# Kernel tuning notes

Measured on AMD Instinct MI355X. Metric: run time of the kernel, lower is better.

Reference implementation:

```python
import jax, jax.numpy as jnp
import numpy as np


def setup_inputs() -> dict:
    key = jax.random.key(0)
    k1, k2, k3, k4 = jax.random.split(key, 4)
    B, C, H, W = 4, 256, 48, 48
    scale = 1.0 / np.sqrt(C)  # conv-like init scale
    x = jax.random.normal(k1, (B, C, H, W), dtype=jnp.float32)
    wq = jax.random.normal(k2, (C, C), dtype=jnp.float32) * scale
    wk = jax.random.normal(k3, (C, C), dtype=jnp.float32) * scale
    wv = jax.random.normal(k4, (C, C), dtype=jnp.float32) * scale
    return {"x": x, "wq": wq, "wk": wk, "wv": wv}


def reference(x, wq, wk, wv):
    B, C, H, W = x.shape
    num_heads = 8
    d_k = C // num_heads
    N = H * W

    # 1x1 convs (bias=False) are channel-mixing matmuls: [out_c, in_c]
    def proj(w):
        y = jnp.einsum('oc,bchw->bohw', w, x)
        # view(B, heads, d_k, H*W)
        return y.reshape(B, num_heads, d_k, N)

    q = proj(wq)  # [B, h, d_k, N]
    k = proj(wk)
    v = proj(wv)

    # scores = q^T k / sqrt(d_k) -> [B, h, N, N]
    scores = jnp.einsum('bhdn,bhdm->bhnm', q, k) / jnp.sqrt(jnp.asarray(d_k, x.dtype))
    attn = jax.nn.softmax(scores, axis=-1)
    # out = attn @ v^T -> [B, h, N, d_k]
    out = jnp.einsum('bhnm,bhdm->bhnd', attn, v)
    # permute back to [B, h, d_k, N] then view(B, C, H, W)
    out = out.transpose(0, 1, 3, 2).reshape(B, C, H, W)
    return x + out
```

## Files before the change

### kernel.cpp

```cpp
#include <hip/hip_runtime.h>

constexpr int B  = 4;
constexpr int C  = 256;
constexpr int N  = 2304;
constexpr int NH = 8;
constexpr int DK = 32;

typedef short short8 __attribute__((ext_vector_type(8)));
typedef float f32x4  __attribute__((ext_vector_type(4)));

static __device__ __forceinline__ ushort f2bf(float f) {
    union { float f; unsigned u; } v; v.f = f;
    unsigned r = (v.u + 0x7FFFu + ((v.u >> 16) & 1u)) >> 16;
    return (ushort)r;
}

__global__ __launch_bounds__(256) void proj_kernel(
    const float* __restrict__ x,
    const float* __restrict__ wq,
    const float* __restrict__ wk,
    const float* __restrict__ wv,
    ushort* __restrict__ ws,
    int bfix, size_t matStride, size_t batchStride)
{
    const int tile = blockIdx.x;
    const int mat  = blockIdx.y;
    const int b    = (bfix >= 0) ? bfix : (int)blockIdx.z;
    const int nt = tile % (N / 64);
    const int ot = tile / (N / 64);
    const int n0 = nt * 64;
    const int o0 = ot * 64;

    const float* w = (mat == 0) ? wq : (mat == 1) ? wk : wv;
    ushort* out = ws + (size_t)mat * matStride + (size_t)b * batchStride;
    const float* xb = x + (size_t)b * C * N;

    __shared__ float xs[16][64];
    __shared__ float wt[64][17];

    const int tid = threadIdx.x;
    const int tx = tid & 15;
    const int ty = tid >> 4;

    float acc[4][4] = {};

    for (int k0 = 0; k0 < C; k0 += 16) {
        {
            const int kk  = tid >> 4;
            const int nn4 = tid & 15;
            float4 v = *reinterpret_cast<const float4*>(xb + (size_t)(k0 + kk) * N + n0 + nn4 * 4);
            *reinterpret_cast<float4*>(&xs[kk][nn4 * 4]) = v;
        }
        {
            const int oo = tid >> 2;
            const int k4 = tid & 3;
            float4 v = *reinterpret_cast<const float4*>(w + (size_t)(o0 + oo) * C + k0 + k4 * 4);
            wt[oo][k4 * 4 + 0] = v.x;
            wt[oo][k4 * 4 + 1] = v.y;
            wt[oo][k4 * 4 + 2] = v.z;
            wt[oo][k4 * 4 + 3] = v.w;
        }
        __syncthreads();

        #pragma unroll
        for (int kk = 0; kk < 16; ++kk) {
            float4 a = *reinterpret_cast<const float4*>(&xs[kk][tx * 4]);
            float av[4] = {a.x, a.y, a.z, a.w};
            float bv[4];
            #pragma unroll
            for (int jo = 0; jo < 4; ++jo) bv[jo] = wt[ty * 4 + jo][kk];
            #pragma unroll
            for (int jo = 0; jo < 4; ++jo)
                #pragma unroll
                for (int jn = 0; jn < 4; ++jn)
                    acc[jo][jn] = fmaf(bv[jo], av[jn], acc[jo][jn]);
        }
        __syncthreads();
    }

    const float sc = (mat == 0) ? 0.17677669529663687f : 1.0f;
    #pragma unroll
    for (int jn = 0; jn < 4; ++jn) {
        ushort4 wv4 = make_ushort4(f2bf(acc[0][jn] * sc), f2bf(acc[1][jn] * sc),
                                   f2bf(acc[2][jn] * sc), f2bf(acc[3][jn] * sc));
        *reinterpret_cast<ushort4*>(out + (size_t)(n0 + tx * 4 + jn) * C + o0 + ty * 4) = wv4;
    }
}

__global__ __launch_bounds__(256) void attn_kernel(
    const ushort* __restrict__ ws,
    const float* __restrict__ x,
    float* __restrict__ out,
    int bfix, size_t matStride, size_t batchStride, int ppx)
{
    __shared__ __align__(16) char smem[18944];
    ushort* Ks  = (ushort*)smem;
    ushort* Vt  = (ushort*)(smem + 5120);
    float*  Ost = (float*) smem;

    const int tid = threadIdx.x;
    const int wq = tid >> 6;
    const int l  = tid & 63;
    const int lq = l & 15;
    const int g  = l >> 4;

    ushort* Pl = (ushort*)(smem + 9728) + wq * 1152;

    const int gid  = blockIdx.x;
    const int xcd  = gid & 7;
    const int loc  = gid >> 3;
    const int pair = xcd * ppx + loc / 36;
    const int qt   = loc % 36;
    const int h    = pair & 7;
    const int b    = (bfix >= 0) ? bfix : (pair >> 3);
    const int n0   = qt * 64;

    const ushort* qb = ws + (size_t)b * batchStride;
    const ushort* kb = qb + matStride;
    const ushort* vb = qb + 2 * matStride;

    short8 qf = *reinterpret_cast<const short8*>(
        qb + (size_t)(n0 + wq * 16 + lq) * C + h * DK + 8 * g);

    f32x4 acc0 = {0.f, 0.f, 0.f, 0.f};
    f32x4 acc1 = {0.f, 0.f, 0.f, 0.f};
    float m = -1e30f, lsum = 0.f;

    const int srow = tid >> 2, sch = tid & 3;
    const int kp = tid & 31, dg = tid >> 5;

    for (int m0 = 0; m0 < N; m0 += 64) {
        *reinterpret_cast<short8*>(Ks + srow * 40 + sch * 8) =
            *reinterpret_cast<const short8*>(kb + (size_t)(m0 + srow) * C + h * DK + sch * 8);
        {
            const ushort* v0 = vb + (size_t)(m0 + 2 * kp) * C + h * DK + dg * 4;
            ushort4 a  = *reinterpret_cast<const ushort4*>(v0);
            ushort4 c4 = *reinterpret_cast<const ushort4*>(v0 + C);
            *reinterpret_cast<unsigned*>(Vt + (dg * 4 + 0) * 72 + 2 * kp) = (unsigned)a.x | ((unsigned)c4.x << 16);
            *reinterpret_cast<unsigned*>(Vt + (dg * 4 + 1) * 72 + 2 * kp) = (unsigned)a.y | ((unsigned)c4.y << 16);
            *reinterpret_cast<unsigned*>(Vt + (dg * 4 + 2) * 72 + 2 * kp) = (unsigned)a.z | ((unsigned)c4.z << 16);
            *reinterpret_cast<unsigned*>(Vt + (dg * 4 + 3) * 72 + 2 * kp) = (unsigned)a.w | ((unsigned)c4.w << 16);
        }
        __syncthreads();

        f32x4 st[4];
        #pragma unroll
        for (int t = 0; t < 4; ++t) {
            short8 kf = *reinterpret_cast<const short8*>(Ks + (lq + 16 * t) * 40 + 8 * g);
            f32x4 z = {0.f, 0.f, 0.f, 0.f};
            st[t] = __builtin_amdgcn_mfma_f32_16x16x32_bf16(kf, qf, z, 0, 0, 0);
        }

        float mx = st[0][0];
        #pragma unroll
        for (int t = 0; t < 4; ++t)
            #pragma unroll
            for (int r = 0; r < 4; ++r) mx = fmaxf(mx, st[t][r]);
        mx = fmaxf(mx, __shfl_xor(mx, 16));
        mx = fmaxf(mx, __shfl_xor(mx, 32));
        const float newm = fmaxf(m, mx);
        const float corr = __expf(m - newm);
        m = newm;

        float ps = 0.f;
        ushort pb[16];
        #pragma unroll
        for (int t = 0; t < 4; ++t)
            #pragma unroll
            for (int r = 0; r < 4; ++r) {
                float p = __expf(st[t][r] - m);
                ps += p;
                pb[t * 4 + r] = f2bf(p);
            }
        ps += __shfl_xor(ps, 16);
        ps += __shfl_xor(ps, 32);
        lsum = lsum * corr + ps;

        float cw[4];
        #pragma unroll
        for (int r = 0; r < 4; ++r) cw[r] = __shfl(corr, 4 * g + r);
        #pragma unroll
        for (int r = 0; r < 4; ++r) { acc0[r] *= cw[r]; acc1[r] *= cw[r]; }

        #pragma unroll
        for (int t = 0; t < 4; ++t) {
            ushort4 w4 = make_ushort4(pb[4 * t], pb[4 * t + 1], pb[4 * t + 2], pb[4 * t + 3]);
            *reinterpret_cast<ushort4*>(Pl + lq * 72 + 4 * g + 16 * t) = w4;
        }

        short8 pf0 = *reinterpret_cast<const short8*>(Pl + lq * 72 + 8 * g);
        short8 pf1 = *reinterpret_cast<const short8*>(Pl + lq * 72 + 32 + 8 * g);
        #pragma unroll
        for (int kc = 0; kc < 2; ++kc) {
            short8 pf = kc ? pf1 : pf0;
            short8 vf0 = *reinterpret_cast<const short8*>(Vt + lq * 72 + 32 * kc + 8 * g);
            short8 vf1 = *reinterpret_cast<const short8*>(Vt + (lq + 16) * 72 + 32 * kc + 8 * g);
            acc0 = __builtin_amdgcn_mfma_f32_16x16x32_bf16(pf, vf0, acc0, 0, 0, 0);
            acc1 = __builtin_amdgcn_mfma_f32_16x16x32_bf16(pf, vf1, acc1, 0, 0, 0);
        }
        __syncthreads();
    }

    const float iv = 1.0f / lsum;
    float iw[4];
    #pragma unroll
    for (int r = 0; r < 4; ++r) iw[r] = __shfl(iv, 4 * g + r);
    #pragma unroll
    for (int r = 0; r < 4; ++r) {
        Ost[(lq +  0) * 68 + wq * 16 + 4 * g + r] = acc0[r] * iw[r];
        Ost[(lq + 16) * 68 + wq * 16 + 4 * g + r] = acc1[r] * iw[r];
    }
    __syncthreads();

    {
        const int d  = tid >> 3;
        const int nn = (tid & 7) * 8;
        const size_t go = ((size_t)b * C + h * DK + d) * (size_t)N + n0 + nn;
        float4 o1 = *reinterpret_cast<float4*>(Ost + d * 68 + nn);
        float4 o2 = *reinterpret_cast<float4*>(Ost + d * 68 + nn + 4);
        float4 x1 = *reinterpret_cast<const float4*>(x + go);
        float4 x2 = *reinterpret_cast<const float4*>(x + go + 4);
        *reinterpret_cast<float4*>(out + go)     = make_float4(o1.x + x1.x, o1.y + x1.y, o1.z + x1.z, o1.w + x1.w);
        *reinterpret_cast<float4*>(out + go + 4) = make_float4(o2.x + x2.x, o2.y + x2.y, o2.z + x2.z, o2.w + x2.w);
    }
}

extern "C" void kernel_launch(void* const* d_in, const int* in_sizes, int n_in,
                              void* d_out, int out_size, void* d_ws, size_t ws_size,
                              hipStream_t stream) {
    const float* x  = (const float*)d_in[0];
    const float* wq = (const float*)d_in[1];
    const float* wk = (const float*)d_in[2];
    const float* wv = (const float*)d_in[3];
    float* out = (float*)d_out;
    ushort* ws = (ushort*)d_ws;

    const size_t NC = (size_t)N * C;
    const size_t needFull = 3 * (size_t)B * NC * sizeof(ushort);

    if (ws_size >= needFull) {
        proj_kernel<<<dim3((N / 64) * (C / 64), 3, B), 256, 0, stream>>>(
            x, wq, wk, wv, ws, -1, (size_t)B * NC, NC);
        attn_kernel<<<dim3(36 * NH * B), 256, 0, stream>>>(
            ws, x, out, -1, (size_t)B * NC, NC, 4);
    } else {
        for (int b = 0; b < B; ++b) {
            proj_kernel<<<dim3((N / 64) * (C / 64), 3, 1), 256, 0, stream>>>(
                x, wq, wk, wv, ws, b, NC, 0);
            attn_kernel<<<dim3(36 * NH), 256, 0, stream>>>(
                ws, x, out, b, NC, 0, 1);
        }
    }
}
```

Before: 232.1 us.

## Shrink attention blocks, prefetch K/V tiles into registers, use exp2 with lazy rescaling

The attention kernel now uses 128-thread blocks covering 32 queries each, which doubles the grid and cuts shared memory per block. The next K/V tile is loaded into registers while the current one is computed, and MFMA sections are wrapped in s_setprio. The softmax switches to exp2 by folding log2(e) into the Q scale, rescales the running max only when a wave's max grows by more than 8, defers the lsum reduction to the end, and uses the v_cvt_pk_bf16_f32 packed convert. In exchange, K/V are read from global once per 32 queries instead of once per 64, doubling that traffic, and the lazy rescale lets intermediate values grow by up to 2^8.

Measured after the change: 229.6 us. No clear change (-1.0%).

```diff
diff --git a/kernel.cpp b/kernel.cpp
--- a/kernel.cpp
+++ b/kernel.cpp
@@ -11,8 +11,12 @@
 
 static __device__ __forceinline__ ushort f2bf(float f) {
     union { float f; unsigned u; } v; v.f = f;
-    unsigned r = (v.u + 0x7FFFu + ((v.u >> 16) & 1u)) >> 16;
-    return (ushort)r;
+    return (ushort)((v.u + 0x7FFFu + ((v.u >> 16) & 1u)) >> 16);
+}
+static __device__ __forceinline__ unsigned cvtpk(float lo, float hi) {
+    unsigned r;
+    asm("v_cvt_pk_bf16_f32 %0, %1, %2" : "=v"(r) : "v"(lo), "v"(hi));
+    return r;
 }
 
 __global__ __launch_bounds__(256) void proj_kernel(
@@ -26,10 +30,8 @@
     const int tile = blockIdx.x;
     const int mat  = blockIdx.y;
     const int b    = (bfix >= 0) ? bfix : (int)blockIdx.z;
-    const int nt = tile % (N / 64);
-    const int ot = tile / (N / 64);
-    const int n0 = nt * 64;
-    const int o0 = ot * 64;
+    const int n0 = (tile % (N / 64)) * 64;
+    const int o0 = (tile / (N / 64)) * 64;
 
     const float* w = (mat == 0) ? wq : (mat == 1) ? wk : wv;
     ushort* out = ws + (size_t)mat * matStride + (size_t)b * batchStride;
@@ -78,7 +80,7 @@
         __syncthreads();
     }
 
-    const float sc = (mat == 0) ? 0.17677669529663687f : 1.0f;
+    const float sc = (mat == 0) ? 0.25503450535f : 1.0f;
     #pragma unroll
     for (int jn = 0; jn < 4; ++jn) {
         ushort4 wv4 = make_ushort4(f2bf(acc[0][jn] * sc), f2bf(acc[1][jn] * sc),
@@ -87,33 +89,33 @@
     }
 }
 
-__global__ __launch_bounds__(256) void attn_kernel(
+__global__ __launch_bounds__(128) void attn_kernel(
     const ushort* __restrict__ ws,
     const float* __restrict__ x,
     float* __restrict__ out,
     int bfix, size_t matStride, size_t batchStride, int ppx)
 {
-    __shared__ __align__(16) char smem[18944];
+    __shared__ __align__(16) char smem[14336];
     ushort* Ks  = (ushort*)smem;
     ushort* Vt  = (ushort*)(smem + 5120);
     float*  Ost = (float*) smem;
 
     const int tid = threadIdx.x;
-    const int wq = tid >> 6;
-    const int l  = tid & 63;
-    const int lq = l & 15;
-    const int g  = l >> 4;
+    const int wq  = tid >> 6;
+    const int l   = tid & 63;
+    const int lq  = l & 15;
+    const int g   = l >> 4;
 
     ushort* Pl = (ushort*)(smem + 9728) + wq * 1152;
 
     const int gid  = blockIdx.x;
     const int xcd  = gid & 7;
     const int loc  = gid >> 3;
-    const int pair = xcd * ppx + loc / 36;
-    const int qt   = loc % 36;
+    const int pair = xcd * ppx + loc / 72;
+    const int qt   = loc % 72;
     const int h    = pair & 7;
     const int b    = (bfix >= 0) ? bfix : (pair >> 3);
-    const int n0   = qt * 64;
+    const int n0   = qt * 32;
 
     const ushort* qb = ws + (size_t)b * batchStride;
     const ushort* kb = qb + matStride;
@@ -126,98 +128,139 @@
     f32x4 acc1 = {0.f, 0.f, 0.f, 0.f};
     float m = -1e30f, lsum = 0.f;
 
-    const int srow = tid >> 2, sch = tid & 3;
-    const int kp = tid & 31, dg = tid >> 5;
-
-    for (int m0 = 0; m0 < N; m0 += 64) {
-        *reinterpret_cast<short8*>(Ks + srow * 40 + sch * 8) =
-            *reinterpret_cast<const short8*>(kb + (size_t)(m0 + srow) * C + h * DK + sch * 8);
+    const int kr = tid >> 2, kc = tid & 3;
+    const int vp = tid & 31, vd = tid >> 5;
+
+    short8  kreg0, kreg1;
+    ushort4 va0, vc0, va1, vc1;
+
+    #define LOAD_TILE(m0_)                                                          \
+        {                                                                           \
+            const int m0i = (m0_);                                                  \
+            kreg0 = *reinterpret_cast<const short8*>(kb + (size_t)(m0i + kr) * C + h * DK + kc * 8);        \
+            kreg1 = *reinterpret_cast<const short8*>(kb + (size_t)(m0i + 32 + kr) * C + h * DK + kc * 8);   \
+            const ushort* v0 = vb + (size_t)(m0i + 2 * vp) * C + h * DK + vd * 4;   \
+            va0 = *reinterpret_cast<const ushort4*>(v0);                            \
+            vc0 = *reinterpret_cast<const ushort4*>(v0 + C);                        \
+            va1 = *reinterpret_cast<const ushort4*>(v0 + 16);                       \
+            vc1 = *reinterpret_cast<const ushort4*>(v0 + C + 16);                   \
+        }
+
+    LOAD_TILE(0);
+
+    for (int t = 0; t < N / 64; ++t) {
+        *reinterpret_cast<short8*>(Ks + kr * 40 + kc * 8) = kreg0;
+        *reinterpret_cast<short8*>(Ks + (kr + 32) * 40 + kc * 8) = kreg1;
         {
-            const ushort* v0 = vb + (size_t)(m0 + 2 * kp) * C + h * DK + dg * 4;
-            ushort4 a  = *reinterpret_cast<const ushort4*>(v0);
-            ushort4 c4 = *reinterpret_cast<const ushort4*>(v0 + C);
-            *reinterpret_cast<unsigned*>(Vt + (dg * 4 + 0) * 72 + 2 * kp) = (unsigned)a.x | ((unsigned)c4.x << 16);
-            *reinterpret_cast<unsigned*>(Vt + (dg * 4 + 1) * 72 + 2 * kp) = (unsigned)a.y | ((unsigned)c4.y << 16);
-            *reinterpret_cast<unsigned*>(Vt + (dg * 4 + 2) * 72 + 2 * kp) = (unsigned)a.z | ((unsigned)c4.z << 16);
-            *reinterpret_cast<unsigned*>(Vt + (dg * 4 + 3) * 72 + 2 * kp) = (unsigned)a.w | ((unsigned)c4.w << 16);
-        }
-        __syncthreads();
+            unsigned p0 = (unsigned)va0.x | ((unsigned)vc0.x << 16);
+            unsigned p1 = (unsigned)va0.y | ((unsigned)vc0.y << 16);
+            unsigned p2 = (unsigned)va0.z | ((unsigned)vc0.z << 16);
+            unsigned p3 = (unsigned)va0.w | ((unsigned)vc0.w << 16);
+            *reinterpret_cast<unsigned*>(Vt + (vd * 4 + 0) * 72 + 2 * vp) = p0;
+            *reinterpret_cast<unsigned*>(Vt + (vd * 4 + 1) * 72 + 2 * vp) = p1;
+            *reinterpret_cast<unsigned*>(Vt + (vd * 4 + 2) * 72 + 2 * vp) = p2;
+            *reinterpret_cast<unsigned*>(Vt + (vd * 4 + 3) * 72 + 2 * vp) = p3;
+            unsigned q0 = (unsigned)va1.x | ((unsigned)vc1.x << 16);
+            unsigned q1 = (unsigned)va1.y | ((unsigned)vc1.y << 16);
+            unsigned q2 = (unsigned)va1.z | ((unsigned)vc1.z << 16);
+            unsigned q3 = (unsigned)va1.w | ((unsigned)vc1.w << 16);
+            *reinterpret_cast<unsigned*>(Vt + (vd * 4 + 16) * 72 + 2 * vp) = q0;
+            *reinterpret_cast<unsigned*>(Vt + (vd * 4 + 17) * 72 + 2 * vp) = q1;
+            *reinterpret_cast<unsigned*>(Vt + (vd * 4 + 18) * 72 + 2 * vp) = q2;
+            *reinterpret_cast<unsigned*>(Vt + (vd * 4 + 19) * 72 + 2 * vp) = q3;
+        }
+        __syncthreads();
+
+        if (t < N / 64 - 1) LOAD_TILE((t + 1) * 64);
 
         f32x4 st[4];
-        #pragma unroll
-        for (int t = 0; t < 4; ++t) {
-            short8 kf = *reinterpret_cast<const short8*>(Ks + (lq + 16 * t) * 40 + 8 * g);
+        __builtin_amdgcn_s_setprio(1);
+        #pragma unroll
+        for (int u = 0; u < 4; ++u) {
+            short8 kf = *reinterpret_cast<const short8*>(Ks + (lq + 16 * u) * 40 + 8 * g);
             f32x4 z = {0.f, 0.f, 0.f, 0.f};
-            st[t] = __builtin_amdgcn_mfma_f32_16x16x32_bf16(kf, qf, z, 0, 0, 0);
-        }
-
-        float mx = st[0][0];
-        #pragma unroll
-        for (int t = 0; t < 4; ++t)
+            st[u] = __builtin_amdgcn_mfma_f32_16x16x32_bf16(kf, qf, z, 0, 0, 0);
+        }
+        __builtin_amdgcn_s_setprio(0);
+
+        float mxl = st[0][0];
+        #pragma unroll
+        for (int u = 0; u < 4; ++u)
             #pragma unroll
-            for (int r = 0; r < 4; ++r) mx = fmaxf(mx, st[t][r]);
-        mx = fmaxf(mx, __shfl_xor(mx, 16));
-        mx = fmaxf(mx, __shfl_xor(mx, 32));
-        const float newm = fmaxf(m, mx);
-        const float corr = __expf(m - newm);
-        m = newm;
+            for (int r = 0; r < 4; ++r) mxl = fmaxf(mxl, st[u][r]);
+
+        if (!__all(mxl <= m + 8.0f)) {
+            float mx = fmaxf(mxl, __shfl_xor(mxl, 16));
+            mx = fmaxf(mx, __shfl_xor(mx, 32));
+            float nm = fmaxf(m, mx);
+            float corr = exp2f(m - nm);
+            m = nm;
+            lsum *= corr;
+            float cw0 = __shfl(corr, 4 * g + 0);
+            float cw1 = __shfl(corr, 4 * g + 1);
+            float cw2 = __shfl(corr, 4 * g + 2);
+            float cw3 = __shfl(corr, 4 * g + 3);
+            acc0[0] *= cw0; acc0[1] *= cw1; acc0[2] *= cw2; acc0[3] *= cw3;
+            acc1[0] *= cw0; acc1[1] *= cw1; acc1[2] *= cw2; acc1[3] *= cw3;
+        }
 
         float ps = 0.f;
-        ushort pb[16];
-        #pragma unroll
-        for (int t = 0; t < 4; ++t)
-            #pragma unroll
-            for (int r = 0; r < 4; ++r) {
-                float p = __expf(st[t][r] - m);
-                ps += p;
-                pb[t * 4 + r] = f2bf(p);
-            }
-        ps += __shfl_xor(ps, 16);
-        ps += __shfl_xor(ps, 32);
-        lsum = lsum * corr + ps;
-
-        float cw[4];
-        #pragma unroll
-        for (int r = 0; r < 4; ++r) cw[r] = __shfl(corr, 4 * g + r);
-        #pragma unroll
-        for (int r = 0; r < 4; ++r) { acc0[r] *= cw[r]; acc1[r] *= cw[r]; }
-
-        #pragma unroll
-        for (int t = 0; t < 4; ++t) {
-            ushort4 w4 = make_ushort4(pb[4 * t], pb[4 * t + 1], pb[4 * t + 2], pb[4 * t + 3]);
-            *reinterpret_cast<ushort4*>(Pl + lq * 72 + 4 * g + 16 * t) = w4;
-        }
+        uint2 pw[4];
+        #pragma unroll
+        for (int u = 0; u < 4; ++u) {
+            float p0 = exp2f(st[u][0] - m);
+            float p1 = exp2f(st[u][1] - m);
+            float p2 = exp2f(st[u][2] - m);
+            float p3 = exp2f(st[u][3] - m);
+            ps += (p0 + p1) + (p2 + p3);
+            pw[u].x = cvtpk(p0, p1);
+            pw[u].y = cvtpk(p2, p3);
+        }
+        lsum += ps;
+
+        #pragma unroll
+        for (int u = 0; u < 4; ++u)
+            *reinterpret_cast<uint2*>(Pl + lq * 72 + 4 * g + 16 * u) = pw[u];
 
         short8 pf0 = *reinterpret_cast<const short8*>(Pl + lq * 72 + 8 * g);
         short8 pf1 = *reinterpret_cast<const short8*>(Pl + lq * 72 + 32 + 8 * g);
-        #pragma unroll
-        for (int kc = 0; kc < 2; ++kc) {
-            short8 pf = kc ? pf1 : pf0;
-            short8 vf0 = *reinterpret_cast<const short8*>(Vt + lq * 72 + 32 * kc + 8 * g);
-            short8 vf1 = *reinterpret_cast<const short8*>(Vt + (lq + 16) * 72 + 32 * kc + 8 * g);
+        __builtin_amdgcn_s_setprio(1);
+        #pragma unroll
+        for (int k2 = 0; k2 < 2; ++k2) {
+            short8 pf = k2 ? pf1 : pf0;
+            short8 vf0 = *reinterpret_cast<const short8*>(Vt + lq * 72 + 32 * k2 + 8 * g);
+            short8 vf1 = *reinterpret_cast<const short8*>(Vt + (lq + 16) * 72 + 32 * k2 + 8 * g);
             acc0 = __builtin_amdgcn_mfma_f32_16x16x32_bf16(pf, vf0, acc0, 0, 0, 0);
             acc1 = __builtin_amdgcn_mfma_f32_16x16x32_bf16(pf, vf1, acc1, 0, 0, 0);
         }
-        __syncthreads();
-    }
-
+        __builtin_amdgcn_s_setprio(0);
+        __syncthreads();
+    }
+
+    lsum += __shfl_xor(lsum, 16);
+    lsum += __shfl_xor(lsum, 32);
     const float iv = 1.0f / lsum;
-    float iw[4];
-    #pragma unroll
-    for (int r = 0; r < 4; ++r) iw[r] = __shfl(iv, 4 * g + r);
-    #pragma unroll
-    for (int r = 0; r < 4; ++r) {
-        Ost[(lq +  0) * 68 + wq * 16 + 4 * g + r] = acc0[r] * iw[r];
-        Ost[(lq + 16) * 68 + wq * 16 + 4 * g + r] = acc1[r] * iw[r];
-    }
+    float iw0 = __shfl(iv, 4 * g + 0);
+    float iw1 = __shfl(iv, 4 * g + 1);
+    float iw2 = __shfl(iv, 4 * g + 2);
+    float iw3 = __shfl(iv, 4 * g + 3);
+
+    Ost[(lq +  0) * 36 + wq * 16 + 4 * g + 0] = acc0[0] * iw0;
+    Ost[(lq +  0) * 36 + wq * 16 + 4 * g + 1] = acc0[1] * iw1;
+    Ost[(lq +  0) * 36 + wq * 16 + 4 * g + 2] = acc0[2] * iw2;
+    Ost[(lq +  0) * 36 + wq * 16 + 4 * g + 3] = acc0[3] * iw3;
+    Ost[(lq + 16) * 36 + wq * 16 + 4 * g + 0] = acc1[0] * iw0;
+    Ost[(lq + 16) * 36 + wq * 16 + 4 * g + 1] = acc1[1] * iw1;
+    Ost[(lq + 16) * 36 + wq * 16 + 4 * g + 2] = acc1[2] * iw2;
+    Ost[(lq + 16) * 36 + wq * 16 + 4 * g + 3] = acc1[3] * iw3;
     __syncthreads();
 
     {
-        const int d  = tid >> 3;
-        const int nn = (tid & 7) * 8;
+        const int d  = tid >> 2;
+        const int nn = (tid & 3) * 8;
         const size_t go = ((size_t)b * C + h * DK + d) * (size_t)N + n0 + nn;
-        float4 o1 = *reinterpret_cast<float4*>(Ost + d * 68 + nn);
-        float4 o2 = *reinterpret_cast<float4*>(Ost + d * 68 + nn + 4);
+        float4 o1 = *reinterpret_cast<float4*>(Ost + d * 36 + nn);
+        float4 o2 = *reinterpret_cast<float4*>(Ost + d * 36 + nn + 4);
         float4 x1 = *reinterpret_cast<const float4*>(x + go);
         float4 x2 = *reinterpret_cast<const float4*>(x + go + 4);
         *reinterpret_cast<float4*>(out + go)     = make_float4(o1.x + x1.x, o1.y + x1.y, o1.z + x1.z, o1.w + x1.w);
@@ -241,13 +284,13 @@
     if (ws_size >= needFull) {
         proj_kernel<<<dim3((N / 64) * (C / 64), 3, B), 256, 0, stream>>>(
             x, wq, wk, wv, ws, -1, (size_t)B * NC, NC);
-        attn_kernel<<<dim3(36 * NH * B), 256, 0, stream>>>(
+        attn_kernel<<<dim3(72 * NH * B), 128, 0, stream>>>(
             ws, x, out, -1, (size_t)B * NC, NC, 4);
     } else {
         for (int b = 0; b < B; ++b) {
             proj_kernel<<<dim3((N / 64) * (C / 64), 3, 1), 256, 0, stream>>>(
                 x, wq, wk, wv, ws, b, NC, 0);
-            attn_kernel<<<dim3(36 * NH), 256, 0, stream>>>(
+            attn_kernel<<<dim3(72 * NH), 128, 0, stream>>>(
                 ws, x, out, b, NC, 0, 1);
         }
     }
```
